# Performance work log

Measured on AMD Instinct MI355X. Metric: run time of the kernel, lower is better.

Reference implementation:

```python
import jax, jax.numpy as jnp
import numpy as np

N = 100000   # nodes
H = 128      # hidden_channels == in_channels (residual requires equality)
H2 = 64      # hidden_channels // 2 (per-sign half)
E = 800000   # edges per sign
LN_EPS = 1e-5


def setup_inputs() -> dict:
    key = jax.random.key(0)
    ks = jax.random.split(key, 32)
    def rn(k, shape, s=0.05):
        return jax.random.normal(k, shape, jnp.float32) * s
    return {
        "x": rn(ks[0], (N, H), 1.0),
        "pos_edge_index": jax.random.randint(ks[1], (2, E), 0, N, jnp.int32),
        "neg_edge_index": jax.random.randint(ks[2], (2, E), 0, N, jnp.int32),
        # SignedConv layer 0 (first_aggr=True): lin_*_l (no bias), lin_*_r (bias)
        "c0_pl_w": rn(ks[3], (H2, H)), "c0_pr_w": rn(ks[4], (H2, H)), "c0_pr_b": rn(ks[5], (H2,)),
        "c0_nl_w": rn(ks[6], (H2, H)), "c0_nr_w": rn(ks[7], (H2, H)), "c0_nr_b": rn(ks[8], (H2,)),
        # SignedConv layer 1 (first_aggr=False): lin_*_l maps 2*H2 -> H2
        "c1_pl_w": rn(ks[9], (H2, 2 * H2)), "c1_pr_w": rn(ks[10], (H2, H2)), "c1_pr_b": rn(ks[11], (H2,)),
        "c1_nl_w": rn(ks[12], (H2, 2 * H2)), "c1_nr_w": rn(ks[13], (H2, H2)), "c1_nr_b": rn(ks[14], (H2,)),
        # LayerNorms
        "ln0_g": 1.0 + rn(ks[15], (H,)), "ln0_b": rn(ks[16], (H,)),
        "ln1_g": 1.0 + rn(ks[17], (H,)), "ln1_b": rn(ks[18], (H,)),
        # proj head: Linear -> GELU -> Linear
        "pw1": rn(ks[19], (H, H)), "pb1": rn(ks[20], (H,)),
        "pw2": rn(ks[21], (H, H)), "pb2": rn(ks[22], (H,)),
        "gate": jnp.array(0.5, jnp.float32),
    }


def _mean_aggr(feat, edge_index, n_nodes):
    """Mean of source features over incoming edges at each target node."""
    src, dst = edge_index[0], edge_index[1]
    msg = feat[src]                                           # [E, F] gather
    s = jax.ops.segment_sum(msg, dst, num_segments=n_nodes)   # [N, F] scatter-add
    cnt = jax.ops.segment_sum(jnp.ones_like(dst, feat.dtype), dst, num_segments=n_nodes)
    return s / jnp.clip(cnt, 1.0)[:, None]


def _layer_norm(x, g, b):
    mu = jnp.mean(x, axis=-1, keepdims=True)
    var = jnp.mean(jnp.square(x - mu), axis=-1, keepdims=True)
    return (x - mu) * jax.lax.rsqrt(var + LN_EPS) * g + b


def reference(x, pos_edge_index, neg_edge_index,
              c0_pl_w, c0_pr_w, c0_pr_b, c0_nl_w, c0_nr_w, c0_nr_b,
              c1_pl_w, c1_pr_w, c1_pr_b, c1_nl_w, c1_nr_w, c1_nr_b,
              ln0_g, ln0_b, ln1_g, ln1_b, pw1, pb1, pw2, pb2, gate):
    n = x.shape[0]
    x0 = x
    # ---- SignedConv layer 0 (first_aggr=True) ----
    ap = _mean_aggr(x, pos_edge_index, n)
    an = _mean_aggr(x, neg_edge_index, n)
    out_pos = ap @ c0_pl_w.T + x @ c0_pr_w.T + c0_pr_b
    out_neg = an @ c0_nl_w.T + x @ c0_nr_w.T + c0_nr_b
    h = jnp.concatenate([out_pos, out_neg], axis=-1)          # [N, H]
    h = _layer_norm(jax.nn.relu(h), ln0_g, ln0_b)             # dropout: eval (identity)
    # ---- SignedConv layer 1 (first_aggr=False) ----
    xp, xn = h[:, :H2], h[:, H2:]
    pos_msg = jnp.concatenate([_mean_aggr(xp, pos_edge_index, n),
                               _mean_aggr(xn, neg_edge_index, n)], axis=-1)  # [N, 2*H2]
    neg_msg = jnp.concatenate([_mean_aggr(xn, pos_edge_index, n),
                               _mean_aggr(xp, neg_edge_index, n)], axis=-1)
    out_pos = pos_msg @ c1_pl_w.T + xp @ c1_pr_w.T + c1_pr_b
    out_neg = neg_msg @ c1_nl_w.T + xn @ c1_nr_w.T + c1_nr_b
    h = jnp.concatenate([out_pos, out_neg], axis=-1)
    h = _layer_norm(jax.nn.relu(h), ln1_g, ln1_b)
    # ---- proj head + gated residual ----
    h = jax.nn.gelu(h @ pw1.T + pb1, approximate=False) @ pw2.T + pb2
    return gate * h + (1.0 - gate) * x0
```

## Files before the change

### kernel.cpp

```cpp
#include <hip/hip_runtime.h>
#include <cstddef>

#define NN 100000
#define HH 128
#define EE 800000

typedef __attribute__((ext_vector_type(8))) short bf16x8;
typedef __attribute__((ext_vector_type(4))) float f32x4;


__device__ __forceinline__ short f2bf(float f){
  union { float f; unsigned u; } x; x.f = f;
  unsigned r = (x.u + 0x7FFFu + ((x.u >> 16) & 1u)) >> 16;
  return (short)r;
}

__device__ __forceinline__ float gelu_f(float v){
  return 0.5f * v * (1.0f + erff(v * 0.70710678118654752f));
}

__device__ __forceinline__ float red16(float s){
  s += __shfl_xor(s, 1);
  s += __shfl_xor(s, 2);
  s += __shfl_xor(s, 4);
  s += __shfl_xor(s, 8);
  return s;
}

__device__ __forceinline__ bf16x8 load_afrag(const float* __restrict__ src, int row, int kq, bool valid){
  bf16x8 a;
  if (valid){
    float4 v0 = *(const float4*)(src + (size_t)row * HH + kq);
    float4 v1 = *(const float4*)(src + (size_t)row * HH + kq + 4);
    a[0]=f2bf(v0.x); a[1]=f2bf(v0.y); a[2]=f2bf(v0.z); a[3]=f2bf(v0.w);
    a[4]=f2bf(v1.x); a[5]=f2bf(v1.y); a[6]=f2bf(v1.z); a[7]=f2bf(v1.w);
  } else {
    #pragma unroll
    for (int i = 0; i < 8; ++i) a[i] = 0;
  }
  return a;
}

__device__ __forceinline__ void mfma_phase64(const float* __restrict__ src, int arow, bool valid,
    int col_off, const short* __restrict__ Bp, f32x4* acc, int lr, int q){
  #pragma unroll
  for (int kc = 0; kc < 2; ++kc){
    int kq = col_off + kc*32 + q*8;
    int kb = kc*4 + q;
    bf16x8 a = load_afrag(src, arow, kq, valid);
    #pragma unroll
    for (int ct = 0; ct < 4; ++ct){
      bf16x8 b = *(const bf16x8*)(Bp + (size_t)(kb*64 + ct*16 + lr)*8);
      acc[ct] = __builtin_amdgcn_mfma_f32_16x16x32_bf16(a, b, acc[ct], 0, 0, 0);
    }
  }
}

__device__ __forceinline__ void ln_epi(f32x4* accP, f32x4* accN,
    const float* __restrict__ biasP, const float* __restrict__ biasN,
    const float* __restrict__ g, const float* __restrict__ b,
    float* __restrict__ out, int base_row, int lr, int q)
{
  float bp[4], bn[4], gp[4], gn[4], b0p[4], b0n[4];
  #pragma unroll
  for (int ct = 0; ct < 4; ++ct){
    int c = ct*16 + lr;
    bp[ct] = biasP[c];  bn[ct] = biasN[c];
    gp[ct] = g[c];      gn[ct] = g[64 + c];
    b0p[ct] = b[c];     b0n[ct] = b[64 + c];
  }
  #pragma unroll
  for (int i = 0; i < 4; ++i){
    int node = base_row + 4*q + i;
    float vP[4], vN[4];
    float s = 0.f;
    #pragma unroll
    for (int ct = 0; ct < 4; ++ct){
      vP[ct] = fmaxf(accP[ct][i] + bp[ct], 0.f);
      vN[ct] = fmaxf(accN[ct][i] + bn[ct], 0.f);
      s += vP[ct] + vN[ct];
    }
    s = red16(s);
    float mu = s * (1.0f / 128.0f);
    float q2 = 0.f;
    #pragma unroll
    for (int ct = 0; ct < 4; ++ct){
      float dP = vP[ct] - mu, dN = vN[ct] - mu;
      q2 += dP*dP + dN*dN;
    }
    q2 = red16(q2);
    float rstd = rsqrtf(q2 * (1.0f / 128.0f) + 1e-5f);
    if (node < NN){
      #pragma unroll
      for (int ct = 0; ct < 4; ++ct){
        int c = ct*16 + lr;
        out[(size_t)node * HH + c]      = (vP[ct] - mu) * rstd * gp[ct] + b0p[ct];
        out[(size_t)node * HH + 64 + c] = (vN[ct] - mu) * rstd * gn[ct] + b0n[ct];
      }
    }
  }
}


__global__ void hist_kernel(const int* __restrict__ pe, const int* __restrict__ ne,
                            int* __restrict__ cnt_p, int* __restrict__ cnt_n){
  int t = blockIdx.x * 256 + threadIdx.x;
  if (t < EE)            atomicAdd(&cnt_p[pe[EE + t]], 1);
  else if (t < 2 * EE)   atomicAdd(&cnt_n[ne[EE + (t - EE)]], 1);
}

__global__ void scan1_kernel(const int* __restrict__ cnt_p, const int* __restrict__ cnt_n,
                             int* __restrict__ off_p, int* __restrict__ off_n,
                             int* __restrict__ parts){
  __shared__ int sh[256];
  const int arr = blockIdx.y;
  const int* cnt = arr ? cnt_n : cnt_p;
  int* off = arr ? off_n : off_p;
  const int b = blockIdx.x, t = threadIdx.x;
  const int base = b * 1024 + t * 4;
  int4 v = make_int4(0, 0, 0, 0);
  if (base + 3 < NN) v = *(const int4*)(cnt + base);
  else {
    if (base + 0 < NN) v.x = cnt[base + 0];
    if (base + 1 < NN) v.y = cnt[base + 1];
    if (base + 2 < NN) v.z = cnt[base + 2];
  }
  int s = v.x + v.y + v.z + v.w;
  sh[t] = s; __syncthreads();
  for (int d = 1; d < 256; d <<= 1){
    int tv = (t >= d) ? sh[t - d] : 0;
    __syncthreads();
    sh[t] += tv;
    __syncthreads();
  }
  int excl = sh[t] - s;
  if (base + 0 < NN) off[base + 0] = excl;
  if (base + 1 < NN) off[base + 1] = excl + v.x;
  if (base + 2 < NN) off[base + 2] = excl + v.x + v.y;
  if (base + 3 < NN) off[base + 3] = excl + v.x + v.y + v.z;
  if (t == 255) parts[arr * 128 + b] = sh[255];
}

__global__ void scan2_kernel(int* __restrict__ parts){
  int t = threadIdx.x;
  if (t < 2){
    int run = 0;
    for (int b = 0; b < 98; ++b){ int v = parts[t * 128 + b]; parts[t * 128 + b] = run; run += v; }
  }
}

__global__ void scan3_kernel(const int* __restrict__ parts,
                             const int* __restrict__ cnt_p, const int* __restrict__ cnt_n,
                             int* __restrict__ off_p, int* __restrict__ off_n,
                             int* __restrict__ cur_p, int* __restrict__ cur_n,
                             float* __restrict__ rp, float* __restrict__ rn){
  const int arr = blockIdx.y;
  int i = blockIdx.x * 256 + threadIdx.x;
  if (i < NN){
    if (arr == 0){
      int o = off_p[i] + parts[i >> 10];
      off_p[i] = o; cur_p[i] = o;
      rp[i] = 1.0f / fmaxf((float)cnt_p[i], 1.0f);
    } else {
      int o = off_n[i] + parts[128 + (i >> 10)];
      off_n[i] = o; cur_n[i] = o;
      rn[i] = 1.0f / fmaxf((float)cnt_n[i], 1.0f);
    }
  }
  if (blockIdx.x == 0 && threadIdx.x == 0){
    if (arr == 0) off_p[NN] = EE; else off_n[NN] = EE;
  }
}

__global__ void scatter_kernel(const int* __restrict__ pe, const int* __restrict__ ne,
                               int* __restrict__ cur_p, int* __restrict__ cur_n,
                               int* __restrict__ srcp, int* __restrict__ srcn){
  int t = blockIdx.x * 256 + threadIdx.x;
  if (t < EE){
    int p = atomicAdd(&cur_p[pe[EE + t]], 1);
    srcp[p] = pe[t];
  } else if (t < 2 * EE){
    int u = t - EE;
    int p = atomicAdd(&cur_n[ne[EE + u]], 1);
    srcn[p] = ne[u];
  }
}


__global__ __launch_bounds__(256) void agg_gather_kernel(const float* __restrict__ feat,
    const int* __restrict__ srcp, const int* __restrict__ srcn,
    const int* __restrict__ off_p, const int* __restrict__ off_n,
    const float* __restrict__ rp, const float* __restrict__ rn,
    float* __restrict__ sp, float* __restrict__ sn){
  int wid  = (blockIdx.x * 256 + threadIdx.x) >> 6;
  int lane = threadIdx.x & 63;
  if (wid >= 2 * NN) return;
  int nidx; const int* srcl; const int* off; const float* rcp; float* outp;
  if (wid < NN){ nidx = wid;      srcl = srcp; off = off_p; rcp = rp; outp = sp; }
  else         { nidx = wid - NN; srcl = srcn; off = off_n; rcp = rn; outp = sn; }
  int j = off[nidx], e = off[nidx + 1];
  const int fo = lane * 2;
  float ax[8], ay[8];
  #pragma unroll
  for (int i = 0; i < 8; ++i){ ax[i] = 0.f; ay[i] = 0.f; }
  for (; j + 7 < e; j += 8){
    #pragma unroll
    for (int i = 0; i < 8; ++i){
      int s = srcl[j + i];
      float2 v = *(const float2*)(feat + (size_t)s * HH + fo);
      ax[i] += v.x; ay[i] += v.y;
    }
  }
  if (j + 3 < e){
    #pragma unroll
    for (int i = 0; i < 4; ++i){
      int s = srcl[j + i];
      float2 v = *(const float2*)(feat + (size_t)s * HH + fo);
      ax[i] += v.x; ay[i] += v.y;
    }
    j += 4;
  }
  if (j + 1 < e){
    #pragma unroll
    for (int i = 0; i < 2; ++i){
      int s = srcl[j + i];
      float2 v = *(const float2*)(feat + (size_t)s * HH + fo);
      ax[i] += v.x; ay[i] += v.y;
    }
    j += 2;
  }
  if (j < e){
    int s = srcl[j];
    float2 v = *(const float2*)(feat + (size_t)s * HH + fo);
    ax[0] += v.x; ay[0] += v.y;
  }
  float r = rcp[nidx];
  float2 o;
  o.x = (((ax[0]+ax[1])+(ax[2]+ax[3])) + ((ax[4]+ax[5])+(ax[6]+ax[7]))) * r;
  o.y = (((ay[0]+ay[1])+(ay[2]+ay[3])) + ((ay[4]+ay[5])+(ay[6]+ay[7]))) * r;
  *(float2*)(outp + (size_t)nidx * HH + fo) = o;
}


__global__ void prep_kernel(const float* __restrict__ c0_pl, const float* __restrict__ c0_pr,
                            const float* __restrict__ c0_nl, const float* __restrict__ c0_nr,
                            const float* __restrict__ c1_pl, const float* __restrict__ c1_pr,
                            const float* __restrict__ c1_nl, const float* __restrict__ c1_nr,
                            const float* __restrict__ pw1, const float* __restrict__ pw2,
                            short* __restrict__ WTb){
  int t = blockIdx.x * 256 + threadIdx.x;
  if (t >= 90112) return;
  int rb, N, k, j; float val;
  if (t < 8192){        rb = 0;     N = 64;  int u = t;         k = u >> 6; j = u & 63;  val = c0_pl[j*128 + k]; }
  else if (t < 16384){  rb = 8192;  N = 64;  int u = t - 8192;  k = u >> 6; j = u & 63;  val = c0_nl[j*128 + k]; }
  else if (t < 32768){  rb = 16384; N = 128; int u = t - 16384; k = u >> 7; j = u & 127;
                        val = (j < 64) ? c0_pr[j*128 + k] : c0_nr[(j-64)*128 + k]; }
  else if (t < 36864){  rb = 32768; N = 64;  int u = t - 32768; k = u >> 6; j = u & 63;  val = c1_pl[j*128 + k]; }
  else if (t < 40960){  rb = 36864; N = 64;  int u = t - 36864; k = u >> 6; j = u & 63;  val = c1_nl[j*128 + k]; }
  else if (t < 45056){  rb = 40960; N = 64;  int u = t - 40960; k = u >> 6; j = u & 63;  val = c1_nl[j*128 + 64 + k]; }
  else if (t < 49152){  rb = 45056; N = 64;  int u = t - 45056; k = u >> 6; j = u & 63;  val = c1_pl[j*128 + 64 + k]; }
  else if (t < 53248){  rb = 49152; N = 64;  int u = t - 49152; k = u >> 6; j = u & 63;  val = c1_pr[j*64 + k]; }
  else if (t < 57344){  rb = 53248; N = 64;  int u = t - 53248; k = u >> 6; j = u & 63;  val = c1_nr[j*64 + k]; }
  else if (t < 73728){  rb = 57344; N = 128; int u = t - 57344; k = u >> 7; j = u & 127; val = pw1[j*128 + k]; }
  else {                rb = 73728; N = 128; int u = t - 73728; k = u >> 7; j = u & 127; val = pw2[j*128 + k]; }
  WTb[rb + ((k >> 3) * N + j) * 8 + (k & 7)] = f2bf(val);
}


__global__ __launch_bounds__(256) void l0_kernel(
    const float* __restrict__ x, const float* __restrict__ sp, const float* __restrict__ sn,
    const short* __restrict__ WTb,
    const float* __restrict__ biasP, const float* __restrict__ biasN,
    const float* __restrict__ lng, const float* __restrict__ lnb,
    float* __restrict__ h0)
{
  const int l = threadIdx.x & 63, w = threadIdx.x >> 6;
  const int lr = l & 15, q = l >> 4;
  const int base_row = (blockIdx.x << 6) + (w << 4);
  const int arow = base_row + lr;
  const bool valid = arow < NN;
  f32x4 accP[4], accN[4];
  #pragma unroll
  for (int ct = 0; ct < 4; ++ct)
    #pragma unroll
    for (int i = 0; i < 4; ++i){ accP[ct][i] = 0.f; accN[ct][i] = 0.f; }

  mfma_phase64(sp, arow, valid, 0,  WTb + 0,    accP, lr, q);
  mfma_phase64(sp, arow, valid, 64, WTb + 4096, accP, lr, q);
  mfma_phase64(sn, arow, valid, 0,  WTb + 8192, accN, lr, q);
  mfma_phase64(sn, arow, valid, 64, WTb + 12288, accN, lr, q);
  #pragma unroll
  for (int kc = 0; kc < 4; ++kc){
    int kq = kc*32 + q*8, kb = kc*4 + q;
    bf16x8 a = load_afrag(x, arow, kq, valid);
    #pragma unroll
    for (int ct = 0; ct < 4; ++ct){
      bf16x8 bp = *(const bf16x8*)(WTb + 16384 + (size_t)(kb*128 + ct*16 + lr)*8);
      bf16x8 bn = *(const bf16x8*)(WTb + 16384 + (size_t)(kb*128 + 64 + ct*16 + lr)*8);
      accP[ct] = __builtin_amdgcn_mfma_f32_16x16x32_bf16(a, bp, accP[ct], 0, 0, 0);
      accN[ct] = __builtin_amdgcn_mfma_f32_16x16x32_bf16(a, bn, accN[ct], 0, 0, 0);
    }
  }
  ln_epi(accP, accN, biasP, biasN, lng, lnb, h0, base_row, lr, q);
}

__global__ __launch_bounds__(256) void l1_kernel(
    const float* __restrict__ h0, const float* __restrict__ sp, const float* __restrict__ sn,
    const short* __restrict__ WTb,
    const float* __restrict__ biasP, const float* __restrict__ biasN,
    const float* __restrict__ lng, const float* __restrict__ lnb,
    float* __restrict__ h1)
{
  const int l = threadIdx.x & 63, w = threadIdx.x >> 6;
  const int lr = l & 15, q = l >> 4;
  const int base_row = (blockIdx.x << 6) + (w << 4);
  const int arow = base_row + lr;
  const bool valid = arow < NN;
  f32x4 accP[4], accN[4];
  #pragma unroll
  for (int ct = 0; ct < 4; ++ct)
    #pragma unroll
    for (int i = 0; i < 4; ++i){ accP[ct][i] = 0.f; accN[ct][i] = 0.f; }

  mfma_phase64(sp, arow, valid, 0,  WTb + 32768, accP, lr, q);
  mfma_phase64(sp, arow, valid, 64, WTb + 36864, accN, lr, q);
  mfma_phase64(sn, arow, valid, 0,  WTb + 40960, accN, lr, q);
  mfma_phase64(sn, arow, valid, 64, WTb + 45056, accP, lr, q);
  mfma_phase64(h0, arow, valid, 0,  WTb + 49152, accP, lr, q);
  mfma_phase64(h0, arow, valid, 64, WTb + 53248, accN, lr, q);

  ln_epi(accP, accN, biasP, biasN, lng, lnb, h1, base_row, lr, q);
}

__global__ __launch_bounds__(256) void mlp_kernel(
    const float* __restrict__ h1, const float* __restrict__ x0,
    const short* __restrict__ WTb, const float* __restrict__ pb1, const float* __restrict__ pb2,
    const float* __restrict__ gate, float* __restrict__ out)
{
  __shared__ __align__(16) short T[64 * 136];
  const int l = threadIdx.x & 63, w = threadIdx.x >> 6;
  const int lr = l & 15, q = l >> 4;
  const int base_row = (blockIdx.x << 6) + (w << 4);
  const int arow = base_row + lr;
  const bool valid = arow < NN;
  f32x4 accP[4], accN[4];
  #pragma unroll
  for (int ct = 0; ct < 4; ++ct)
    #pragma unroll
    for (int i = 0; i < 4; ++i){ accP[ct][i] = 0.f; accN[ct][i] = 0.f; }

  #pragma unroll
  for (int kc = 0; kc < 4; ++kc){
    int kq = kc*32 + q*8, kb = kc*4 + q;
    bf16x8 a = load_afrag(h1, arow, kq, valid);
    #pragma unroll
    for (int ct = 0; ct < 4; ++ct){
      bf16x8 bp = *(const bf16x8*)(WTb + 57344 + (size_t)(kb*128 + ct*16 + lr)*8);
      bf16x8 bn = *(const bf16x8*)(WTb + 57344 + (size_t)(kb*128 + 64 + ct*16 + lr)*8);
      accP[ct] = __builtin_amdgcn_mfma_f32_16x16x32_bf16(a, bp, accP[ct], 0, 0, 0);
      accN[ct] = __builtin_amdgcn_mfma_f32_16x16x32_bf16(a, bn, accN[ct], 0, 0, 0);
    }
  }
  #pragma unroll
  for (int ct = 0; ct < 4; ++ct){
    int c = ct*16 + lr;
    float p1p = pb1[c], p1n = pb1[64 + c];
    #pragma unroll
    for (int i = 0; i < 4; ++i){
      int r = (w << 4) + 4*q + i;
      T[r*136 + c]      = f2bf(gelu_f(accP[ct][i] + p1p));
      T[r*136 + 64 + c] = f2bf(gelu_f(accN[ct][i] + p1n));
    }
  }
  __syncthreads();
  f32x4 aP[4], aN[4];
  #pragma unroll
  for (int ct = 0; ct < 4; ++ct)
    #pragma unroll
    for (int i = 0; i < 4; ++i){ aP[ct][i] = 0.f; aN[ct][i] = 0.f; }
  const int trow = (w << 4) + lr;
  #pragma unroll
  for (int kc = 0; kc < 4; ++kc){
    int kq = kc*32 + q*8, kb = kc*4 + q;
    bf16x8 a = *(const bf16x8*)(&T[trow*136 + kq]);
    #pragma unroll
    for (int ct = 0; ct < 4; ++ct){
      bf16x8 bp = *(const bf16x8*)(WTb + 73728 + (size_t)(kb*128 + ct*16 + lr)*8);
      bf16x8 bn = *(const bf16x8*)(WTb + 73728 + (size_t)(kb*128 + 64 + ct*16 + lr)*8);
      aP[ct] = __builtin_amdgcn_mfma_f32_16x16x32_bf16(a, bp, aP[ct], 0, 0, 0);
      aN[ct] = __builtin_amdgcn_mfma_f32_16x16x32_bf16(a, bn, aN[ct], 0, 0, 0);
    }
  }
  float gt = gate[0], og = 1.0f - gt;
  #pragma unroll
  for (int i = 0; i < 4; ++i){
    int node = base_row + 4*q + i;
    if (node < NN){
      #pragma unroll
      for (int ct = 0; ct < 4; ++ct){
        int c = ct*16 + lr;
        out[(size_t)node*HH + c]      = gt*(aP[ct][i] + pb2[c])      + og*x0[(size_t)node*HH + c];
        out[(size_t)node*HH + 64 + c] = gt*(aN[ct][i] + pb2[64 + c]) + og*x0[(size_t)node*HH + 64 + c];
      }
    }
  }
}


extern "C" void kernel_launch(void* const* d_in, const int* in_sizes, int n_in,
                              void* d_out, int out_size, void* d_ws, size_t ws_size,
                              hipStream_t stream){
  (void)in_sizes; (void)n_in; (void)out_size;
  const float* x     = (const float*)d_in[0];
  const int*   pe    = (const int*)d_in[1];
  const int*   ne    = (const int*)d_in[2];
  const float* c0_pl = (const float*)d_in[3];
  const float* c0_pr = (const float*)d_in[4];
  const float* c0_pr_b = (const float*)d_in[5];
  const float* c0_nl = (const float*)d_in[6];
  const float* c0_nr = (const float*)d_in[7];
  const float* c0_nr_b = (const float*)d_in[8];
  const float* c1_pl = (const float*)d_in[9];
  const float* c1_pr = (const float*)d_in[10];
  const float* c1_pr_b = (const float*)d_in[11];
  const float* c1_nl = (const float*)d_in[12];
  const float* c1_nr = (const float*)d_in[13];
  const float* c1_nr_b = (const float*)d_in[14];
  const float* ln0_g = (const float*)d_in[15];
  const float* ln0_b = (const float*)d_in[16];
  const float* ln1_g = (const float*)d_in[17];
  const float* ln1_b = (const float*)d_in[18];
  const float* pw1   = (const float*)d_in[19];
  const float* pb1   = (const float*)d_in[20];
  const float* pw2   = (const float*)d_in[21];
  const float* pb2   = (const float*)d_in[22];
  const float* gate  = (const float*)d_in[23];
  float* out = (float*)d_out;
  float* ws  = (float*)d_ws;

  float* s_pos = ws;
  float* s_neg = ws + (size_t)NN * HH;
  float* rp    = ws + (size_t)2 * NN * HH;
  float* rn    = rp + NN;
  short* WTb   = (short*)(rn + NN);
  int* cnt_p = (int*)((char*)WTb + 90112 * sizeof(short));
  int* cnt_n = cnt_p + NN;
  int* off_p = cnt_n + NN;
  int* off_n = off_p + NN + 1;
  int* cur_p = off_n + NN + 1;
  int* cur_n = cur_p + NN;
  int* parts = cur_n + NN;
  int* srcp  = parts + 256;
  int* srcn  = srcp + EE;
  const size_t need = (size_t)((char*)(srcn + EE) - (char*)ws);
  if (ws_size < need) return;

  hipMemsetAsync(cnt_p, 0, (size_t)2 * NN * sizeof(int), stream);
  prep_kernel<<<352, 256, 0, stream>>>(c0_pl, c0_pr, c0_nl, c0_nr,
                                       c1_pl, c1_pr, c1_nl, c1_nr, pw1, pw2, WTb);
  hist_kernel<<<(2 * EE) / 256, 256, 0, stream>>>(pe, ne, cnt_p, cnt_n);
  scan1_kernel<<<dim3(98, 2), 256, 0, stream>>>(cnt_p, cnt_n, off_p, off_n, parts);
  scan2_kernel<<<1, 64, 0, stream>>>(parts);
  scan3_kernel<<<dim3(391, 2), 256, 0, stream>>>(parts, cnt_p, cnt_n, off_p, off_n,
                                                 cur_p, cur_n, rp, rn);
  scatter_kernel<<<(2 * EE) / 256, 256, 0, stream>>>(pe, ne, cur_p, cur_n, srcp, srcn);

  agg_gather_kernel<<<(2 * NN * 64) / 256, 256, 0, stream>>>(x, srcp, srcn, off_p, off_n,
                                                             rp, rn, s_pos, s_neg);
  l0_kernel<<<(NN + 63) / 64, 256, 0, stream>>>(x, s_pos, s_neg, WTb,
                                                c0_pr_b, c0_nr_b, ln0_g, ln0_b, out );
  agg_gather_kernel<<<(2 * NN * 64) / 256, 256, 0, stream>>>(out , srcp, srcn, off_p, off_n,
                                                             rp, rn, s_pos, s_neg);
  l1_kernel<<<(NN + 63) / 64, 256, 0, stream>>>(out , s_pos, s_neg, WTb,
                                                c1_pr_b, c1_nr_b, ln1_g, ln1_b, s_pos );
  mlp_kernel<<<(NN + 63) / 64, 256, 0, stream>>>(s_pos , x, WTb, pb1, pb2, gate, out);
}
```

Baseline: 712.2 us.

## Store node features and aggregates in bf16 to halve gather traffic

Converts the input x to bf16 once and keeps every intermediate feature buffer (aggregates, h0, h1) in bf16 instead of fp32. The edge gathers read 4 bytes per lane instead of 8, and the MFMA kernels load bf16 fragments directly with no conversion. This halves the memory traffic of the bandwidth-bound random gathers and the intermediate writes. The cost is an extra conversion kernel and lower precision in the stored activations and aggregated sums.

```diff
diff --git a/kernel.cpp b/kernel.cpp
--- a/kernel.cpp
+++ b/kernel.cpp
@@ -13,6 +13,10 @@
   union { float f; unsigned u; } x; x.f = f;
   unsigned r = (x.u + 0x7FFFu + ((x.u >> 16) & 1u)) >> 16;
   return (short)r;
+}
+
+__device__ __forceinline__ float bf2f(unsigned short us){
+  union { unsigned u; float f; } t; t.u = (unsigned)us << 16; return t.f;
 }
 
 __device__ __forceinline__ float gelu_f(float v){
@@ -27,27 +31,21 @@
   return s;
 }
 
-__device__ __forceinline__ bf16x8 load_afrag(const float* __restrict__ src, int row, int kq, bool valid){
-  bf16x8 a;
-  if (valid){
-    float4 v0 = *(const float4*)(src + (size_t)row * HH + kq);
-    float4 v1 = *(const float4*)(src + (size_t)row * HH + kq + 4);
-    a[0]=f2bf(v0.x); a[1]=f2bf(v0.y); a[2]=f2bf(v0.z); a[3]=f2bf(v0.w);
-    a[4]=f2bf(v1.x); a[5]=f2bf(v1.y); a[6]=f2bf(v1.z); a[7]=f2bf(v1.w);
-  } else {
-    #pragma unroll
-    for (int i = 0; i < 8; ++i) a[i] = 0;
-  }
-  return a;
-}
-
-__device__ __forceinline__ void mfma_phase64(const float* __restrict__ src, int arow, bool valid,
+__device__ __forceinline__ bf16x8 load_afrag_bf(const short* __restrict__ src, int row, int kq, bool valid){
+  if (valid) return *(const bf16x8*)(src + (size_t)row * HH + kq);
+  bf16x8 z;
+  #pragma unroll
+  for (int i = 0; i < 8; ++i) z[i] = 0;
+  return z;
+}
+
+__device__ __forceinline__ void mfma_phase64(const short* __restrict__ src, int arow, bool valid,
     int col_off, const short* __restrict__ Bp, f32x4* acc, int lr, int q){
   #pragma unroll
   for (int kc = 0; kc < 2; ++kc){
     int kq = col_off + kc*32 + q*8;
     int kb = kc*4 + q;
-    bf16x8 a = load_afrag(src, arow, kq, valid);
+    bf16x8 a = load_afrag_bf(src, arow, kq, valid);
     #pragma unroll
     for (int ct = 0; ct < 4; ++ct){
       bf16x8 b = *(const bf16x8*)(Bp + (size_t)(kb*64 + ct*16 + lr)*8);
@@ -59,7 +57,7 @@
 __device__ __forceinline__ void ln_epi(f32x4* accP, f32x4* accN,
     const float* __restrict__ biasP, const float* __restrict__ biasN,
     const float* __restrict__ g, const float* __restrict__ b,
-    float* __restrict__ out, int base_row, int lr, int q)
+    short* __restrict__ out, int base_row, int lr, int q)
 {
   float bp[4], bn[4], gp[4], gn[4], b0p[4], b0n[4];
   #pragma unroll
@@ -94,11 +92,23 @@
       #pragma unroll
       for (int ct = 0; ct < 4; ++ct){
         int c = ct*16 + lr;
-        out[(size_t)node * HH + c]      = (vP[ct] - mu) * rstd * gp[ct] + b0p[ct];
-        out[(size_t)node * HH + 64 + c] = (vN[ct] - mu) * rstd * gn[ct] + b0n[ct];
+        out[(size_t)node * HH + c]      = f2bf((vP[ct] - mu) * rstd * gp[ct] + b0p[ct]);
+        out[(size_t)node * HH + 64 + c] = f2bf((vN[ct] - mu) * rstd * gn[ct] + b0n[ct]);
       }
     }
   }
+}
+
+
+__global__ void cvt_kernel(const float* __restrict__ in, short* __restrict__ outb){
+  int i = blockIdx.x * 256 + threadIdx.x;
+  if (i >= (NN * HH) / 8) return;
+  const float4* p = (const float4*)(in + (size_t)i * 8);
+  float4 v0 = p[0], v1 = p[1];
+  bf16x8 o;
+  o[0]=f2bf(v0.x); o[1]=f2bf(v0.y); o[2]=f2bf(v0.z); o[3]=f2bf(v0.w);
+  o[4]=f2bf(v1.x); o[5]=f2bf(v1.y); o[6]=f2bf(v1.z); o[7]=f2bf(v1.w);
+  *(bf16x8*)(outb + (size_t)i * 8) = o;
 }
 
 
@@ -187,15 +197,15 @@
 }
 
 
-__global__ __launch_bounds__(256) void agg_gather_kernel(const float* __restrict__ feat,
+__global__ __launch_bounds__(256) void agg_gather_kernel(const short* __restrict__ feat,
     const int* __restrict__ srcp, const int* __restrict__ srcn,
     const int* __restrict__ off_p, const int* __restrict__ off_n,
     const float* __restrict__ rp, const float* __restrict__ rn,
-    float* __restrict__ sp, float* __restrict__ sn){
+    short* __restrict__ sp, short* __restrict__ sn){
   int wid  = (blockIdx.x * 256 + threadIdx.x) >> 6;
   int lane = threadIdx.x & 63;
   if (wid >= 2 * NN) return;
-  int nidx; const int* srcl; const int* off; const float* rcp; float* outp;
+  int nidx; const int* srcl; const int* off; const float* rcp; short* outp;
   if (wid < NN){ nidx = wid;      srcl = srcp; off = off_p; rcp = rp; outp = sp; }
   else         { nidx = wid - NN; srcl = srcn; off = off_n; rcp = rn; outp = sn; }
   int j = off[nidx], e = off[nidx + 1];
@@ -207,16 +217,18 @@
     #pragma unroll
     for (int i = 0; i < 8; ++i){
       int s = srcl[j + i];
-      float2 v = *(const float2*)(feat + (size_t)s * HH + fo);
-      ax[i] += v.x; ay[i] += v.y;
+      unsigned v = *(const unsigned*)(feat + (size_t)s * HH + fo);
+      ax[i] += bf2f((unsigned short)(v & 0xffffu));
+      ay[i] += bf2f((unsigned short)(v >> 16));
     }
   }
   if (j + 3 < e){
     #pragma unroll
     for (int i = 0; i < 4; ++i){
       int s = srcl[j + i];
-      float2 v = *(const float2*)(feat + (size_t)s * HH + fo);
-      ax[i] += v.x; ay[i] += v.y;
+      unsigned v = *(const unsigned*)(feat + (size_t)s * HH + fo);
+      ax[i] += bf2f((unsigned short)(v & 0xffffu));
+      ay[i] += bf2f((unsigned short)(v >> 16));
     }
     j += 4;
   }
@@ -224,21 +236,23 @@
     #pragma unroll
     for (int i = 0; i < 2; ++i){
       int s = srcl[j + i];
-      float2 v = *(const float2*)(feat + (size_t)s * HH + fo);
-      ax[i] += v.x; ay[i] += v.y;
+      unsigned v = *(const unsigned*)(feat + (size_t)s * HH + fo);
+      ax[i] += bf2f((unsigned short)(v & 0xffffu));
+      ay[i] += bf2f((unsigned short)(v >> 16));
     }
     j += 2;
   }
   if (j < e){
     int s = srcl[j];
-    float2 v = *(const float2*)(feat + (size_t)s * HH + fo);
-    ax[0] += v.x; ay[0] += v.y;
+    unsigned v = *(const unsigned*)(feat + (size_t)s * HH + fo);
+    ax[0] += bf2f((unsigned short)(v & 0xffffu));
+    ay[0] += bf2f((unsigned short)(v >> 16));
   }
   float r = rcp[nidx];
-  float2 o;
-  o.x = (((ax[0]+ax[1])+(ax[2]+ax[3])) + ((ax[4]+ax[5])+(ax[6]+ax[7]))) * r;
-  o.y = (((ay[0]+ay[1])+(ay[2]+ay[3])) + ((ay[4]+ay[5])+(ay[6]+ay[7]))) * r;
-  *(float2*)(outp + (size_t)nidx * HH + fo) = o;
+  float ox = (((ax[0]+ax[1])+(ax[2]+ax[3])) + ((ax[4]+ax[5])+(ax[6]+ax[7]))) * r;
+  float oy = (((ay[0]+ay[1])+(ay[2]+ay[3])) + ((ay[4]+ay[5])+(ay[6]+ay[7]))) * r;
+  unsigned ov = ((unsigned)(unsigned short)f2bf(oy) << 16) | (unsigned)(unsigned short)f2bf(ox);
+  *(unsigned*)(outp + (size_t)nidx * HH + fo) = ov;
 }
 
 
@@ -268,11 +282,11 @@
 
 
 __global__ __launch_bounds__(256) void l0_kernel(
-    const float* __restrict__ x, const float* __restrict__ sp, const float* __restrict__ sn,
+    const short* __restrict__ xb, const short* __restrict__ sp, const short* __restrict__ sn,
     const short* __restrict__ WTb,
     const float* __restrict__ biasP, const float* __restrict__ biasN,
     const float* __restrict__ lng, const float* __restrict__ lnb,
-    float* __restrict__ h0)
+    short* __restrict__ h0)
 {
   const int l = threadIdx.x & 63, w = threadIdx.x >> 6;
   const int lr = l & 15, q = l >> 4;
@@ -285,14 +299,14 @@
     #pragma unroll
     for (int i = 0; i < 4; ++i){ accP[ct][i] = 0.f; accN[ct][i] = 0.f; }
 
-  mfma_phase64(sp, arow, valid, 0,  WTb + 0,    accP, lr, q);
-  mfma_phase64(sp, arow, valid, 64, WTb + 4096, accP, lr, q);
-  mfma_phase64(sn, arow, valid, 0,  WTb + 8192, accN, lr, q);
+  mfma_phase64(sp, arow, valid, 0,  WTb + 0,     accP, lr, q);
+  mfma_phase64(sp, arow, valid, 64, WTb + 4096,  accP, lr, q);
+  mfma_phase64(sn, arow, valid, 0,  WTb + 8192,  accN, lr, q);
   mfma_phase64(sn, arow, valid, 64, WTb + 12288, accN, lr, q);
   #pragma unroll
   for (int kc = 0; kc < 4; ++kc){
     int kq = kc*32 + q*8, kb = kc*4 + q;
-    bf16x8 a = load_afrag(x, arow, kq, valid);
+    bf16x8 a = load_afrag_bf(xb, arow, kq, valid);
     #pragma unroll
     for (int ct = 0; ct < 4; ++ct){
       bf16x8 bp = *(const bf16x8*)(WTb + 16384 + (size_t)(kb*128 + ct*16 + lr)*8);
@@ -305,11 +319,11 @@
 }
 
 __global__ __launch_bounds__(256) void l1_kernel(
-    const float* __restrict__ h0, const float* __restrict__ sp, const float* __restrict__ sn,
+    const short* __restrict__ h0, const short* __restrict__ sp, const short* __restrict__ sn,
     const short* __restrict__ WTb,
     const float* __restrict__ biasP, const float* __restrict__ biasN,
     const float* __restrict__ lng, const float* __restrict__ lnb,
-    float* __restrict__ h1)
+    short* __restrict__ h1)
 {
   const int l = threadIdx.x & 63, w = threadIdx.x >> 6;
   const int lr = l & 15, q = l >> 4;
@@ -333,7 +347,7 @@
 }
 
 __global__ __launch_bounds__(256) void mlp_kernel(
-    const float* __restrict__ h1, const float* __restrict__ x0,
+    const short* __restrict__ h1, const float* __restrict__ x0,
     const short* __restrict__ WTb, const float* __restrict__ pb1, const float* __restrict__ pb2,
     const float* __restrict__ gate, float* __restrict__ out)
 {
@@ -352,7 +366,7 @@
   #pragma unroll
   for (int kc = 0; kc < 4; ++kc){
     int kq = kc*32 + q*8, kb = kc*4 + q;
-    bf16x8 a = load_afrag(h1, arow, kq, valid);
+    bf16x8 a = load_afrag_bf(h1, arow, kq, valid);
     #pragma unroll
     for (int ct = 0; ct < 4; ++ct){
       bf16x8 bp = *(const bf16x8*)(WTb + 57344 + (size_t)(kb*128 + ct*16 + lr)*8);
@@ -436,14 +450,15 @@
   const float* pb2   = (const float*)d_in[22];
   const float* gate  = (const float*)d_in[23];
   float* out = (float*)d_out;
-  float* ws  = (float*)d_ws;
-
-  float* s_pos = ws;
-  float* s_neg = ws + (size_t)NN * HH;
-  float* rp    = ws + (size_t)2 * NN * HH;
+
+  short* x_bf  = (short*)d_ws;
+  short* s_pos = x_bf + (size_t)NN * HH;
+  short* s_neg = s_pos + (size_t)NN * HH;
+  short* h0    = s_neg + (size_t)NN * HH;
+  float* rp    = (float*)(h0 + (size_t)NN * HH);
   float* rn    = rp + NN;
   short* WTb   = (short*)(rn + NN);
-  int* cnt_p = (int*)((char*)WTb + 90112 * sizeof(short));
+  int* cnt_p = (int*)(WTb + 90112);
   int* cnt_n = cnt_p + NN;
   int* off_p = cnt_n + NN;
   int* off_n = off_p + NN + 1;
@@ -452,10 +467,11 @@
   int* parts = cur_n + NN;
   int* srcp  = parts + 256;
   int* srcn  = srcp + EE;
-  const size_t need = (size_t)((char*)(srcn + EE) - (char*)ws);
+  const size_t need = (size_t)((char*)(srcn + EE) - (char*)d_ws);
   if (ws_size < need) return;
 
   hipMemsetAsync(cnt_p, 0, (size_t)2 * NN * sizeof(int), stream);
+  cvt_kernel<<<(NN * HH / 8 + 255) / 256, 256, 0, stream>>>(x, x_bf);
   prep_kernel<<<352, 256, 0, stream>>>(c0_pl, c0_pr, c0_nl, c0_nr,
                                        c1_pl, c1_pr, c1_nl, c1_nr, pw1, pw2, WTb);
   hist_kernel<<<(2 * EE) / 256, 256, 0, stream>>>(pe, ne, cnt_p, cnt_n);
@@ -465,13 +481,13 @@
                                                  cur_p, cur_n, rp, rn);
   scatter_kernel<<<(2 * EE) / 256, 256, 0, stream>>>(pe, ne, cur_p, cur_n, srcp, srcn);
 
-  agg_gather_kernel<<<(2 * NN * 64) / 256, 256, 0, stream>>>(x, srcp, srcn, off_p, off_n,
+  agg_gather_kernel<<<(2 * NN * 64) / 256, 256, 0, stream>>>(x_bf, srcp, srcn, off_p, off_n,
                                                              rp, rn, s_pos, s_neg);
-  l0_kernel<<<(NN + 63) / 64, 256, 0, stream>>>(x, s_pos, s_neg, WTb,
-                                                c0_pr_b, c0_nr_b, ln0_g, ln0_b, out );
-  agg_gather_kernel<<<(2 * NN * 64) / 256, 256, 0, stream>>>(out , srcp, srcn, off_p, off_n,
+  l0_kernel<<<(NN + 63) / 64, 256, 0, stream>>>(x_bf, s_pos, s_neg, WTb,
+                                                c0_pr_b, c0_nr_b, ln0_g, ln0_b, h0);
+  agg_gather_kernel<<<(2 * NN * 64) / 256, 256, 0, stream>>>(h0, srcp, srcn, off_p, off_n,
                                                              rp, rn, s_pos, s_neg);
-  l1_kernel<<<(NN + 63) / 64, 256, 0, stream>>>(out , s_pos, s_neg, WTb,
+  l1_kernel<<<(NN + 63) / 64, 256, 0, stream>>>(h0, s_pos, s_neg, WTb,
                                                 c1_pr_b, c1_nr_b, ln1_g, ln1_b, s_pos );
   mlp_kernel<<<(NN + 63) / 64, 256, 0, stream>>>(s_pos , x, WTb, pb1, pb2, gate, out);
 }
```

Measured after the change: 605.3 us. -15.0%, faster.
